# Performance work log

Hardware: AMD Instinct MI355X
Metric: run time of the kernel (lower is better)

The kernel has to match this reference:

```python
import jax, jax.numpy as jnp
import numpy as np

C = 512
M = 8            # n_heads
G = 32           # GroupNorm groups
EPS = 1e-6


def setup_inputs() -> dict:
    key = jax.random.key(0)
    ks = jax.random.split(key, 7)
    x = jax.random.normal(ks[0], (2, C, 64, 64), dtype=jnp.float32)
    gn_weight = jnp.ones((C,), jnp.float32)
    gn_bias = jnp.zeros((C,), jnp.float32)
    qkv_w = jax.random.normal(ks[1], (3 * C, C), jnp.float32) * (1.0 / np.sqrt(C))
    qkv_b = jnp.zeros((3 * C,), jnp.float32)
    # source zero-inits proj_out; we use small random weights so the attention
    proj_w = jax.random.normal(ks[2], (C, C), jnp.float32) * (0.02 / np.sqrt(C))
    proj_b = jnp.zeros((C,), jnp.float32)
    return {"x": x, "gn_weight": gn_weight, "gn_bias": gn_bias,
            "qkv_w": qkv_w, "qkv_b": qkv_b, "proj_w": proj_w, "proj_b": proj_b}


def _forward(x, gn_weight, gn_bias, qkv_w, qkv_b, proj_w, proj_b):
    b, c, H, W = x.shape
    n = H * W
    d = c // M
    xf = x.reshape(b, c, n)

    # GroupNorm(32, c, eps=1e-6, affine)
    xg = xf.reshape(b, G, (c // G) * n)
    mu = xg.mean(axis=-1, keepdims=True)
    var = xg.var(axis=-1, keepdims=True)
    xn = ((xg - mu) * jax.lax.rsqrt(var + EPS)).reshape(b, c, n)
    xn = xn * gn_weight[None, :, None] + gn_bias[None, :, None]

    # 1x1 conv -> qkv, then legacy reshape-then-split
    qkv = jnp.einsum('oc,bcn->bon', qkv_w, xn) + qkv_b[None, :, None]  # (b, 3c, n)
    qkv = qkv.reshape(b * M, 3 * d, n)
    q, k, v = qkv[:, :d], qkv[:, d:2 * d], qkv[:, 2 * d:]

    scale = 1.0 / np.sqrt(np.sqrt(d))
    w = jnp.einsum('Bdi,Bdj->Bij', q * scale, k * scale)  # (b*m, n, n)
    w = jax.nn.softmax(w, axis=-1)
    a = jnp.einsum('Bin,Bdn->Bdi', w, v)                  # (b*m, d, n)
    a = a.reshape(b, c, n)

    h = jnp.einsum('oc,bcn->bon', proj_w, a) + proj_b[None, :, None]
    # NOTE: source reassigns x = norm(x) before the residual add.
    return (xn + h).reshape(b, c, H, W)


def reference(x, gn_weight, gn_bias, qkv_w, qkv_b, proj_w, proj_b):
    return _forward(x, gn_weight, gn_bias, qkv_w, qkv_b, proj_w, proj_b)
```

## Files before the change

### kernel.cpp

```cpp
#include <hip/hip_runtime.h>
#include <cstdint>
#include <cstddef>

typedef __attribute__((ext_vector_type(8))) short short8;
typedef __attribute__((ext_vector_type(4))) float f32x4;

#define QSCALE 0.18033688011112043f

__device__ __forceinline__ float bf2f(unsigned short u) {
  return __uint_as_float(((unsigned)u) << 16);
}
__device__ __forceinline__ unsigned short f2bf(float f) {
  unsigned u = __float_as_uint(f);
  u += 0x7fffu + ((u >> 16) & 1u);
  return (unsigned short)(u >> 16);
}
__device__ __forceinline__ unsigned cvtpk(float a, float b) {
  unsigned r;
  asm("v_cvt_pk_bf16_f32 %0, %1, %2" : "=v"(r) : "v"(a), "v"(b));
  return r;
}
__device__ __forceinline__ short8 mk8(unsigned a, unsigned b, unsigned c, unsigned d) {
  union { unsigned u[4]; short8 s; } x;
  x.u[0] = a; x.u[1] = b; x.u[2] = c; x.u[3] = d;
  return x.s;
}
__device__ __forceinline__ void g2l16(const void* g, void* l) {
  __builtin_amdgcn_global_load_lds(
      (const __attribute__((address_space(1))) unsigned int*)g,
      (__attribute__((address_space(3))) unsigned int*)l, 16, 0, 0);
}

__global__ __launch_bounds__(256) void k_wgn(const float* __restrict__ wqf,
                                             const float* __restrict__ wpf,
                                             unsigned short* __restrict__ wq,
                                             unsigned short* __restrict__ wp,
                                             const float* __restrict__ x,
                                             float* __restrict__ part) {
  __shared__ float red[8];
  const int blk = blockIdx.x;
  const int t = threadIdx.x;
  if (blk < 1024) {
    int i = blk * 256 + t;
    if (i < 196608) {
      float4 v = ((const float4*)wqf)[i];
      ushort4 u;
      u.x = f2bf(v.x); u.y = f2bf(v.y); u.z = f2bf(v.z); u.w = f2bf(v.w);
      ((ushort4*)wq)[i] = u;
    } else {
      int k = i - 196608;
      float4 v = ((const float4*)wpf)[k];
      ushort4 u;
      u.x = f2bf(v.x); u.y = f2bf(v.y); u.z = f2bf(v.z); u.w = f2bf(v.w);
      ((ushort4*)wp)[k] = u;
    }
  } else {
    int b2 = blk - 1024;
    int bg = b2 >> 4, slice = b2 & 15;
    const float4* base = (const float4*)(x + (size_t)bg * 65536 + (size_t)slice * 4096);
    float s = 0.f, q = 0.f;
#pragma unroll
    for (int i = 0; i < 4; ++i) {
      float4 v = base[t + i * 256];
      s += v.x + v.y + v.z + v.w;
      q += v.x * v.x + v.y * v.y + v.z * v.z + v.w * v.w;
    }
#pragma unroll
    for (int off = 1; off < 64; off <<= 1) {
      s += __shfl_xor(s, off);
      q += __shfl_xor(q, off);
    }
    int wid = t >> 6;
    if ((t & 63) == 0) { red[wid * 2] = s; red[wid * 2 + 1] = q; }
    __syncthreads();
    if (t == 0) {
      float S = red[0] + red[2] + red[4] + red[6];
      float Q = red[1] + red[3] + red[5] + red[7];
      part[b2 * 2] = S;
      part[b2 * 2 + 1] = Q;
    }
  }
}

__global__ void k_gnfin(const float* __restrict__ part, float* __restrict__ stats) {
  int t = threadIdx.x;
  float S = 0.f, Q = 0.f;
#pragma unroll
  for (int i = 0; i < 16; ++i) {
    S += part[(t * 16 + i) * 2];
    Q += part[(t * 16 + i) * 2 + 1];
  }
  float mean = S * (1.f / 65536.f);
  float var = Q * (1.f / 65536.f) - mean * mean;
  stats[t * 2] = mean;
  stats[t * 2 + 1] = rsqrtf(var + 1e-6f);
}

__global__ __launch_bounds__(256) void k_gnnorm(const float* __restrict__ x,
                                                const float* __restrict__ gnw,
                                                const float* __restrict__ gnb,
                                                const float* __restrict__ stats,
                                                unsigned short* __restrict__ xn,
                                                unsigned short* __restrict__ xnT) {
  __shared__ float T[64 * 65];
  const int t = threadIdx.x;
  const int n0 = blockIdx.x * 64, c0 = blockIdx.y * 64, bb = blockIdx.z;
#pragma unroll
  for (int p = 0; p < 4; ++p) {
    int s = p * 256 + t;
    int row = s >> 4, seg = s & 15;
    int c = c0 + row;
    int gi = bb * 32 + (c >> 4);
    float mean = stats[gi * 2], rstd = stats[gi * 2 + 1];
    float gw = gnw[c] * rstd;
    float gb = gnb[c] - mean * gw;
    float4 v = *(const float4*)(x + ((size_t)bb * 512 + c) * 4096 + n0 + seg * 4);
    float f0 = v.x * gw + gb, f1 = v.y * gw + gb, f2 = v.z * gw + gb, f3 = v.w * gw + gb;
    ushort4 u;
    u.x = f2bf(f0); u.y = f2bf(f1); u.z = f2bf(f2); u.w = f2bf(f3);
    *(ushort4*)(xn + ((size_t)bb * 512 + c) * 4096 + n0 + seg * 4) = u;
    T[(seg * 4 + 0) * 65 + row] = f0;
    T[(seg * 4 + 1) * 65 + row] = f1;
    T[(seg * 4 + 2) * 65 + row] = f2;
    T[(seg * 4 + 3) * 65 + row] = f3;
  }
  __syncthreads();
#pragma unroll
  for (int p = 0; p < 4; ++p) {
    int s = p * 256 + t;
    int nl = s >> 4, cs = s & 15;
    float f0 = T[nl * 65 + cs * 4 + 0];
    float f1 = T[nl * 65 + cs * 4 + 1];
    float f2 = T[nl * 65 + cs * 4 + 2];
    float f3 = T[nl * 65 + cs * 4 + 3];
    ushort4 u;
    u.x = f2bf(f0); u.y = f2bf(f1); u.z = f2bf(f2); u.w = f2bf(f3);
    *(ushort4*)(xnT + ((size_t)bb * 4096 + n0 + nl) * 512 + c0 + cs * 4) = u;
  }
}

template <int MODE>
__global__ __launch_bounds__(256) void k_gemm(
    const unsigned short* __restrict__ A,
    const unsigned short* __restrict__ Bt,
    const float* __restrict__ bias,
    unsigned short* __restrict__ outA,
    unsigned short* __restrict__ outT,
    const unsigned short* __restrict__ resid,
    float* __restrict__ outF,
    int Mo) {
  __shared__ char lds[34816];
  const int t = threadIdx.x;
  const int lane = t & 63;
  const int g = lane >> 4, ln = lane & 15;
  const int wid = t >> 6, wr = wid >> 1, wc = wid & 1;
  const int bn0 = blockIdx.x * 128, bm0 = blockIdx.y * 128, bb = blockIdx.z;

  const unsigned short* Ab = A + (size_t)bm0 * 512;
  const unsigned short* Bb = Bt + ((size_t)bb * 4096 + bn0) * 512;

  f32x4 acc[4][4];
#pragma unroll
  for (int m = 0; m < 4; ++m)
#pragma unroll
    for (int n = 0; n < 4; ++n) acc[m][n] = f32x4{0.f, 0.f, 0.f, 0.f};

#pragma unroll 1
  for (int kt = 0; kt < 8; ++kt) {
#pragma unroll
    for (int p = 0; p < 4; ++p) {
      int s = p * 256 + t;
      int row = s >> 3;
      int csg = (s & 7) ^ (row & 7);
      g2l16(Ab + (size_t)row * 512 + kt * 64 + csg * 8,
            &lds[(p * 256 + (t & ~63)) * 16]);
    }
#pragma unroll
    for (int p = 0; p < 4; ++p) {
      int s = p * 256 + t;
      int row = s >> 3;
      int csg = (s & 7) ^ (row & 7);
      g2l16(Bb + (size_t)row * 512 + kt * 64 + csg * 8,
            &lds[16384 + (p * 256 + (t & ~63)) * 16]);
    }
    __syncthreads();
#pragma unroll
    for (int kk = 0; kk < 2; ++kk) {
      short8 af[4], bfr[4];
#pragma unroll
      for (int m = 0; m < 4; ++m) {
        int row = wr * 64 + m * 16 + ln;
        int cs = (kk * 4 + g) ^ (row & 7);
        af[m] = *(const short8*)&lds[row * 128 + cs * 16];
      }
#pragma unroll
      for (int n = 0; n < 4; ++n) {
        int row = wc * 64 + n * 16 + ln;
        int cs = (kk * 4 + g) ^ (row & 7);
        bfr[n] = *(const short8*)&lds[16384 + row * 128 + cs * 16];
      }
      __builtin_amdgcn_s_setprio(1);
#pragma unroll
      for (int m = 0; m < 4; ++m)
#pragma unroll
        for (int n = 0; n < 4; ++n)
          acc[m][n] = __builtin_amdgcn_mfma_f32_16x16x32_bf16(af[m], bfr[n], acc[m][n], 0, 0, 0);
      __builtin_amdgcn_s_setprio(0);
    }
    __syncthreads();
  }

  if (MODE == 0) {
#pragma unroll
    for (int m = 0; m < 4; ++m)
#pragma unroll
      for (int n = 0; n < 4; ++n)
#pragma unroll
        for (int r = 0; r < 4; ++r) {
          int ol = wr * 64 + m * 16 + g * 4 + r;
          int jl = wc * 64 + n * 16 + ln;
          int o = bm0 + ol, j = bn0 + jl;
          float v = acc[m][n][r] + bias[o];
          unsigned short bv = f2bf(v);
          if ((o % 192) >= 128) {
            int jp = (j & ~63) | (j & 32) | ((j & 0xC) << 1) | ((j & 16) >> 2) | (j & 3);
            outA[((size_t)bb * 1536 + o) * 4096 + jp] = bv;
          }
          *(unsigned short*)&lds[jl * 272 + ol * 2] = bv;
        }
    __syncthreads();
#pragma unroll
    for (int p = 0; p < 8; ++p) {
      int s = p * 256 + t;
      int jl = s >> 4, cs = s & 15;
      int oo = bm0 + cs * 8;
      if ((oo % 192) < 128) {
        short8 v = *(const short8*)&lds[jl * 272 + cs * 16];
        *(short8*)&outT[((size_t)bb * 4096 + bn0 + jl) * 1536 + oo] = v;
      }
    }
  } else {
#pragma unroll
    for (int m = 0; m < 4; ++m)
#pragma unroll
      for (int n = 0; n < 4; ++n)
#pragma unroll
        for (int r = 0; r < 4; ++r) {
          int o = bm0 + wr * 64 + m * 16 + g * 4 + r;
          int j = bn0 + wc * 64 + n * 16 + ln;
          size_t idx = ((size_t)bb * 512 + o) * 4096 + j;
          outF[idx] = acc[m][n][r] + bias[o] + bf2f(resid[idx]);
        }
  }
}

__global__ __launch_bounds__(512, 4) void k_attn(const unsigned short* __restrict__ qkv,
                                                 const unsigned short* __restrict__ qkvT,
                                                 unsigned short* __restrict__ aT) {
  __shared__ char lds[49152];
  const int t = threadIdx.x, lane = t & 63;
  const int g = lane >> 4, ln = lane & 15;
  const int wid = t >> 6;
  const int qw = wid >> 1;
  const int jw = wid & 1;
  const int h = blockIdx.y, bb = blockIdx.z;
  const int q0 = blockIdx.x * 128 + qw * 32;

  int kaddr[2][2], vaddr[4];
#pragma unroll
  for (int kk = 0; kk < 2; ++kk)
#pragma unroll
    for (int jf = 0; jf < 2; ++jf) {
      int row = jw * 32 + jf * 16 + ln;
      kaddr[kk][jf] = row * 128 + (((kk * 4 + g) ^ (row & 7)) << 4);
    }
#pragma unroll
  for (int df = 0; df < 4; ++df) {
    int row = df * 16 + ln;
    vaddr[df] = 24576 + row * 128 + (((jw * 4 + g) ^ (row & 7)) << 4);
  }

  const unsigned short* kS;
  const unsigned short* vS;
  int ldst;
  {
    int row = t >> 3, csg = (t & 7) ^ (row & 7);
    kS = qkvT + ((size_t)bb * 4096 + row) * 1536 + 192 * h + 64 + csg * 8;
    vS = qkv + ((size_t)bb * 1536 + 192 * h + 128 + row) * 4096 + csg * 8;
    ldst = (t & ~63) * 16;
  }

  short8 qf[2][2];
#pragma unroll
  for (int qt = 0; qt < 2; ++qt)
#pragma unroll
    for (int kk = 0; kk < 2; ++kk) {
      short8 v = *(const short8*)(qkvT + ((size_t)bb * 4096 + q0 + qt * 16 + ln) * 1536 +
                                  192 * h + kk * 32 + g * 8);
#pragma unroll
      for (int e = 0; e < 8; ++e) {
        float f = bf2f((unsigned short)v[e]) * QSCALE;
        v[e] = (short)f2bf(f);
      }
      qf[qt][kk] = v;
    }

  const short8 onesb = mk8(0x3F803F80u, 0x3F803F80u, 0x3F803F80u, 0x3F803F80u);

  f32x4 acc[2][4];
  f32x4 lacc[2];
#pragma unroll
  for (int qt = 0; qt < 2; ++qt) {
#pragma unroll
    for (int df = 0; df < 4; ++df) acc[qt][df] = f32x4{0.f, 0.f, 0.f, 0.f};
    lacc[qt] = f32x4{0.f, 0.f, 0.f, 0.f};
  }

#pragma unroll
  for (int jt = 0; jt < 2; ++jt) {
    g2l16(kS, &lds[jt * 8192 + ldst]);
    g2l16(vS, &lds[24576 + jt * 8192 + ldst]);
    kS += 64 * 1536;
    vS += 64;
  }

#pragma unroll 3
  for (int jt = 0; jt < 64; ++jt) {
    const int cur = jt % 3;
    const char* Kc = &lds[cur * 8192];
    if (jt < 63) {
      asm volatile("s_waitcnt vmcnt(2) lgkmcnt(0)" ::: "memory");
    } else {
      asm volatile("s_waitcnt vmcnt(0) lgkmcnt(0)" ::: "memory");
    }
    __builtin_amdgcn_s_barrier();
    __builtin_amdgcn_sched_barrier(0);

    if (jt < 62) {
      int nb = (jt + 2) % 3;
      g2l16(kS, &lds[nb * 8192 + ldst]);
      g2l16(vS, &lds[24576 + nb * 8192 + ldst]);
      kS += 64 * 1536;
      vS += 64;
    }

    short8 kf[2][2];
#pragma unroll
    for (int kk = 0; kk < 2; ++kk)
#pragma unroll
      for (int jf = 0; jf < 2; ++jf) kf[kk][jf] = *(const short8*)(Kc + kaddr[kk][jf]);

    const f32x4 zf = f32x4{0.f, 0.f, 0.f, 0.f};
    f32x4 w[2][2];
    __builtin_amdgcn_s_setprio(1);
#pragma unroll
    for (int qt = 0; qt < 2; ++qt)
#pragma unroll
      for (int jf = 0; jf < 2; ++jf)
        w[qt][jf] = __builtin_amdgcn_mfma_f32_16x16x32_bf16(kf[0][jf], qf[qt][0], zf, 0, 0, 0);
#pragma unroll
    for (int qt = 0; qt < 2; ++qt)
#pragma unroll
      for (int jf = 0; jf < 2; ++jf)
        w[qt][jf] = __builtin_amdgcn_mfma_f32_16x16x32_bf16(kf[1][jf], qf[qt][1], w[qt][jf], 0, 0, 0);
    __builtin_amdgcn_s_setprio(0);

    short8 vf[4];
#pragma unroll
    for (int df = 0; df < 4; ++df) vf[df] = *(const short8*)(Kc + vaddr[df]);

#pragma unroll
    for (int qt = 0; qt < 2; ++qt)
#pragma unroll
      for (int jf = 0; jf < 2; ++jf)
#pragma unroll
        for (int r = 0; r < 4; ++r) w[qt][jf][r] = __builtin_amdgcn_exp2f(w[qt][jf][r]);

    short8 pf[2];
#pragma unroll
    for (int qt = 0; qt < 2; ++qt)
      pf[qt] = mk8(cvtpk(w[qt][0][0], w[qt][0][1]),
                   cvtpk(w[qt][0][2], w[qt][0][3]),
                   cvtpk(w[qt][1][0], w[qt][1][1]),
                   cvtpk(w[qt][1][2], w[qt][1][3]));

    __builtin_amdgcn_s_setprio(1);
#pragma unroll
    for (int qt = 0; qt < 2; ++qt) {
#pragma unroll
      for (int df = 0; df < 4; ++df)
        acc[qt][df] = __builtin_amdgcn_mfma_f32_16x16x32_bf16(pf[qt], vf[df], acc[qt][df], 0, 0, 0);
      lacc[qt] = __builtin_amdgcn_mfma_f32_16x16x32_bf16(pf[qt], onesb, lacc[qt], 0, 0, 0);
    }
    __builtin_amdgcn_s_setprio(0);
  }

  __syncthreads();
  float* cb = (float*)lds;
  const int cbase = qw * 2560;
  if (jw == 1) {
#pragma unroll
    for (int qt = 0; qt < 2; ++qt) {
#pragma unroll
      for (int df = 0; df < 4; ++df)
        *(f32x4*)&cb[cbase + ((qt * 4 + df) * 64 + lane) * 4] = acc[qt][df];
      *(f32x4*)&cb[cbase + 2048 + (qt * 64 + lane) * 4] = lacc[qt];
    }
  }
  __syncthreads();
  if (jw == 0) {
#pragma unroll
    for (int qt = 0; qt < 2; ++qt) {
#pragma unroll
      for (int df = 0; df < 4; ++df)
        acc[qt][df] += *(const f32x4*)&cb[cbase + ((qt * 4 + df) * 64 + lane) * 4];
      lacc[qt] += *(const f32x4*)&cb[cbase + 2048 + (qt * 64 + lane) * 4];
    }
#pragma unroll
    for (int qt = 0; qt < 2; ++qt)
#pragma unroll
      for (int r = 0; r < 4; ++r) {
        float inv = 1.f / lacc[qt][r];
        int row = q0 + qt * 16 + g * 4 + r;
#pragma unroll
        for (int df = 0; df < 4; ++df)
          aT[((size_t)bb * 4096 + row) * 512 + h * 64 + df * 16 + ln] =
              f2bf(acc[qt][df][r] * inv);
      }
  }
}

extern "C" void kernel_launch(void* const* d_in, const int* in_sizes, int n_in,
                              void* d_out, int out_size, void* d_ws, size_t ws_size,
                              hipStream_t stream) {
  const float* x     = (const float*)d_in[0];
  const float* gnw   = (const float*)d_in[1];
  const float* gnb   = (const float*)d_in[2];
  const float* qkvw  = (const float*)d_in[3];
  const float* qkvb  = (const float*)d_in[4];
  const float* projw = (const float*)d_in[5];
  const float* projb = (const float*)d_in[6];
  float* out = (float*)d_out;
  char* ws = (char*)d_ws;

  const size_t OFF_WQ   = 0;
  const size_t OFF_WP   = 1572864;
  const size_t OFF_XN   = 2097152;
  const size_t OFF_XNT  = 10485760;
  const size_t OFF_QKV  = 18874368;
  const size_t OFF_QKVT = 44040192;
  const size_t OFF_AT   = 69206016;
  const size_t OFF_PART = 77594624;
  const size_t OFF_STAT = 77602816;

  unsigned short* wq   = (unsigned short*)(ws + OFF_WQ);
  unsigned short* wp   = (unsigned short*)(ws + OFF_WP);
  unsigned short* xn   = (unsigned short*)(ws + OFF_XN);
  unsigned short* xnT  = (unsigned short*)(ws + OFF_XNT);
  unsigned short* qkv  = (unsigned short*)(ws + OFF_QKV);
  unsigned short* qkvT = (unsigned short*)(ws + OFF_QKVT);
  unsigned short* aT   = (unsigned short*)(ws + OFF_AT);
  float* part  = (float*)(ws + OFF_PART);
  float* stats = (float*)(ws + OFF_STAT);

  k_wgn<<<dim3(2048), dim3(256), 0, stream>>>(qkvw, projw, wq, wp, x, part);
  k_gnfin<<<dim3(1), dim3(64), 0, stream>>>(part, stats);
  k_gnnorm<<<dim3(64, 8, 2), dim3(256), 0, stream>>>(x, gnw, gnb, stats, xn, xnT);
  k_gemm<0><<<dim3(32, 12, 2), dim3(256), 0, stream>>>(wq, xnT, qkvb, qkv, qkvT, nullptr, nullptr, 1536);
  k_attn<<<dim3(32, 8, 2), dim3(512), 0, stream>>>(qkv, qkvT, aT);
  k_gemm<1><<<dim3(32, 4, 2), dim3(256), 0, stream>>>(wp, aT, projb, nullptr, nullptr, xn, out, 512);
}
```

Baseline: 125.5 us.

## Software-pipeline attention loop: overlap previous tile's PV MFMAs with current exp2

Peels the first key tile into a prologue and restructures the main loop so that each tile's P·V MFMAs run one iteration late, interleaved with the exp2 of the current tile's scores. The aim is to hide transcendental latency behind matrix-core work and stop the MFMA and VALU phases from running back to back. An epilogue drains the last P·V. This keeps more registers live (pf and vfp across iterations), and the interleaving is pinned by sched_barriers, which may constrain the compiler.

Result: slower. 128.0 us (+2.0%).

```diff
diff --git a/kernel.cpp b/kernel.cpp
--- a/kernel.cpp
+++ b/kernel.cpp
@@ -316,6 +316,9 @@
     lacc[qt] = f32x4{0.f, 0.f, 0.f, 0.f};
   }
 
+  short8 pf[2];
+  short8 vfp[4];
+
 #pragma unroll
   for (int jt = 0; jt < 2; ++jt) {
     g2l16(kS, &lds[jt * 8192 + ldst]);
@@ -324,8 +327,52 @@
     vS += 64;
   }
 
+  {
+    asm volatile("s_waitcnt vmcnt(2)" ::: "memory");
+    __builtin_amdgcn_s_barrier();
+    __builtin_amdgcn_sched_barrier(0);
+    g2l16(kS, &lds[2 * 8192 + ldst]);
+    g2l16(vS, &lds[24576 + 2 * 8192 + ldst]);
+    kS += 64 * 1536;
+    vS += 64;
+    const char* Kc = &lds[0];
+    short8 kf[2][2];
+#pragma unroll
+    for (int kk = 0; kk < 2; ++kk)
+#pragma unroll
+      for (int jf = 0; jf < 2; ++jf) kf[kk][jf] = *(const short8*)(Kc + kaddr[kk][jf]);
+    const f32x4 zf = f32x4{0.f, 0.f, 0.f, 0.f};
+    f32x4 w[2][2];
+    __builtin_amdgcn_s_setprio(1);
+#pragma unroll
+    for (int qt = 0; qt < 2; ++qt)
+#pragma unroll
+      for (int jf = 0; jf < 2; ++jf)
+        w[qt][jf] = __builtin_amdgcn_mfma_f32_16x16x32_bf16(kf[0][jf], qf[qt][0], zf, 0, 0, 0);
+#pragma unroll
+    for (int qt = 0; qt < 2; ++qt)
+#pragma unroll
+      for (int jf = 0; jf < 2; ++jf)
+        w[qt][jf] = __builtin_amdgcn_mfma_f32_16x16x32_bf16(kf[1][jf], qf[qt][1], w[qt][jf], 0, 0, 0);
+    __builtin_amdgcn_s_setprio(0);
+#pragma unroll
+    for (int qt = 0; qt < 2; ++qt)
+#pragma unroll
+      for (int jf = 0; jf < 2; ++jf)
+#pragma unroll
+        for (int r = 0; r < 4; ++r) w[qt][jf][r] = __builtin_amdgcn_exp2f(w[qt][jf][r]);
+#pragma unroll
+    for (int qt = 0; qt < 2; ++qt)
+      pf[qt] = mk8(cvtpk(w[qt][0][0], w[qt][0][1]),
+                   cvtpk(w[qt][0][2], w[qt][0][3]),
+                   cvtpk(w[qt][1][0], w[qt][1][1]),
+                   cvtpk(w[qt][1][2], w[qt][1][3]));
+#pragma unroll
+    for (int df = 0; df < 4; ++df) vfp[df] = *(const short8*)(Kc + vaddr[df]);
+  }
+
 #pragma unroll 3
-  for (int jt = 0; jt < 64; ++jt) {
+  for (int jt = 1; jt < 64; ++jt) {
     const int cur = jt % 3;
     const char* Kc = &lds[cur * 8192];
     if (jt < 63) {
@@ -363,37 +410,43 @@
 #pragma unroll
       for (int jf = 0; jf < 2; ++jf)
         w[qt][jf] = __builtin_amdgcn_mfma_f32_16x16x32_bf16(kf[1][jf], qf[qt][1], w[qt][jf], 0, 0, 0);
+    __builtin_amdgcn_sched_barrier(0);
+
+#pragma unroll
+    for (int s = 0; s < 8; ++s) {
+      int pqt = s >> 2, pdf = s & 3;
+      acc[pqt][pdf] =
+          __builtin_amdgcn_mfma_f32_16x16x32_bf16(pf[pqt], vfp[pdf], acc[pqt][pdf], 0, 0, 0);
+      int e0 = 2 * s, e1 = 2 * s + 1;
+      w[e0 >> 3][(e0 >> 2) & 1][e0 & 3] =
+          __builtin_amdgcn_exp2f(w[e0 >> 3][(e0 >> 2) & 1][e0 & 3]);
+      w[e1 >> 3][(e1 >> 2) & 1][e1 & 3] =
+          __builtin_amdgcn_exp2f(w[e1 >> 3][(e1 >> 2) & 1][e1 & 3]);
+      __builtin_amdgcn_sched_barrier(0);
+    }
+    lacc[0] = __builtin_amdgcn_mfma_f32_16x16x32_bf16(pf[0], onesb, lacc[0], 0, 0, 0);
+    lacc[1] = __builtin_amdgcn_mfma_f32_16x16x32_bf16(pf[1], onesb, lacc[1], 0, 0, 0);
+    __builtin_amdgcn_sched_barrier(0);
     __builtin_amdgcn_s_setprio(0);
-
-    short8 vf[4];
-#pragma unroll
-    for (int df = 0; df < 4; ++df) vf[df] = *(const short8*)(Kc + vaddr[df]);
-
-#pragma unroll
-    for (int qt = 0; qt < 2; ++qt)
-#pragma unroll
-      for (int jf = 0; jf < 2; ++jf)
-#pragma unroll
-        for (int r = 0; r < 4; ++r) w[qt][jf][r] = __builtin_amdgcn_exp2f(w[qt][jf][r]);
-
-    short8 pf[2];
 #pragma unroll
     for (int qt = 0; qt < 2; ++qt)
       pf[qt] = mk8(cvtpk(w[qt][0][0], w[qt][0][1]),
                    cvtpk(w[qt][0][2], w[qt][0][3]),
                    cvtpk(w[qt][1][0], w[qt][1][1]),
                    cvtpk(w[qt][1][2], w[qt][1][3]));
-
-    __builtin_amdgcn_s_setprio(1);
-#pragma unroll
-    for (int qt = 0; qt < 2; ++qt) {
-#pragma unroll
-      for (int df = 0; df < 4; ++df)
-        acc[qt][df] = __builtin_amdgcn_mfma_f32_16x16x32_bf16(pf[qt], vf[df], acc[qt][df], 0, 0, 0);
-      lacc[qt] = __builtin_amdgcn_mfma_f32_16x16x32_bf16(pf[qt], onesb, lacc[qt], 0, 0, 0);
-    }
-    __builtin_amdgcn_s_setprio(0);
-  }
+#pragma unroll
+    for (int df = 0; df < 4; ++df) vfp[df] = *(const short8*)(Kc + vaddr[df]);
+  }
+
+  __builtin_amdgcn_s_setprio(1);
+#pragma unroll
+  for (int qt = 0; qt < 2; ++qt) {
+#pragma unroll
+    for (int df = 0; df < 4; ++df)
+      acc[qt][df] = __builtin_amdgcn_mfma_f32_16x16x32_bf16(pf[qt], vfp[df], acc[qt][df], 0, 0, 0);
+    lacc[qt] = __builtin_amdgcn_mfma_f32_16x16x32_bf16(pf[qt], onesb, lacc[qt], 0, 0, 0);
+  }
+  __builtin_amdgcn_s_setprio(0);
 
   __syncthreads();
   float* cb = (float*)lds;
```

## Give each attention wave 64 query rows with half the waves per block

Applied to the files above, without the earlier changes.

The attention kernel now runs 4 waves (256 threads) per block instead of 8. Each wave handles 64 query rows instead of 32, so every K/V fragment read from LDS feeds twice as many MFMAs. Each thread issues two global-to-LDS loads per tile to keep the same 64-row K/V tile, and the wait counts and cross-wave reduction offsets are adjusted to match. The goal is less LDS read traffic per FLOP. The cost is more accumulator registers per wave and fewer waves to hide latency.

Result: no change. 125.0 us (median of 2 runs) (-0.4%).

```diff
diff --git a/kernel.cpp b/kernel.cpp
--- a/kernel.cpp
+++ b/kernel.cpp
@@ -254,7 +254,7 @@
   }
 }
 
-__global__ __launch_bounds__(512, 4) void k_attn(const unsigned short* __restrict__ qkv,
+__global__ __launch_bounds__(256, 2) void k_attn(const unsigned short* __restrict__ qkv,
                                                  const unsigned short* __restrict__ qkvT,
                                                  unsigned short* __restrict__ aT) {
   __shared__ char lds[49152];
@@ -264,7 +264,7 @@
   const int qw = wid >> 1;
   const int jw = wid & 1;
   const int h = blockIdx.y, bb = blockIdx.z;
-  const int q0 = blockIdx.x * 128 + qw * 32;
+  const int q0 = blockIdx.x * 128 + qw * 64;
 
   int kaddr[2][2], vaddr[4];
 #pragma unroll
@@ -280,19 +280,21 @@
     vaddr[df] = 24576 + row * 128 + (((jw * 4 + g) ^ (row & 7)) << 4);
   }
 
-  const unsigned short* kS;
-  const unsigned short* vS;
-  int ldst;
-  {
-    int row = t >> 3, csg = (t & 7) ^ (row & 7);
-    kS = qkvT + ((size_t)bb * 4096 + row) * 1536 + 192 * h + 64 + csg * 8;
-    vS = qkv + ((size_t)bb * 1536 + 192 * h + 128 + row) * 4096 + csg * 8;
-    ldst = (t & ~63) * 16;
-  }
-
-  short8 qf[2][2];
-#pragma unroll
-  for (int qt = 0; qt < 2; ++qt)
+  const unsigned short* kS[2];
+  const unsigned short* vS[2];
+  int ldst[2];
+#pragma unroll
+  for (int p = 0; p < 2; ++p) {
+    int s = p * 256 + t;
+    int row = s >> 3, csg = (s & 7) ^ (row & 7);
+    kS[p] = qkvT + ((size_t)bb * 4096 + row) * 1536 + 192 * h + 64 + csg * 8;
+    vS[p] = qkv + ((size_t)bb * 1536 + 192 * h + 128 + row) * 4096 + csg * 8;
+    ldst[p] = (p * 256 + (t & ~63)) * 16;
+  }
+
+  short8 qf[4][2];
+#pragma unroll
+  for (int qt = 0; qt < 4; ++qt)
 #pragma unroll
     for (int kk = 0; kk < 2; ++kk) {
       short8 v = *(const short8*)(qkvT + ((size_t)bb * 4096 + q0 + qt * 16 + ln) * 1536 +
@@ -307,10 +309,10 @@
 
   const short8 onesb = mk8(0x3F803F80u, 0x3F803F80u, 0x3F803F80u, 0x3F803F80u);
 
-  f32x4 acc[2][4];
-  f32x4 lacc[2];
-#pragma unroll
-  for (int qt = 0; qt < 2; ++qt) {
+  f32x4 acc[4][4];
+  f32x4 lacc[4];
+#pragma unroll
+  for (int qt = 0; qt < 4; ++qt) {
 #pragma unroll
     for (int df = 0; df < 4; ++df) acc[qt][df] = f32x4{0.f, 0.f, 0.f, 0.f};
     lacc[qt] = f32x4{0.f, 0.f, 0.f, 0.f};
@@ -318,10 +320,13 @@
 
 #pragma unroll
   for (int jt = 0; jt < 2; ++jt) {
-    g2l16(kS, &lds[jt * 8192 + ldst]);
-    g2l16(vS, &lds[24576 + jt * 8192 + ldst]);
-    kS += 64 * 1536;
-    vS += 64;
+#pragma unroll
+    for (int p = 0; p < 2; ++p) {
+      g2l16(kS[p], &lds[jt * 8192 + ldst[p]]);
+      g2l16(vS[p], &lds[24576 + jt * 8192 + ldst[p]]);
+      kS[p] += 64 * 1536;
+      vS[p] += 64;
+    }
   }
 
 #pragma unroll 3
@@ -329,7 +334,7 @@
     const int cur = jt % 3;
     const char* Kc = &lds[cur * 8192];
     if (jt < 63) {
-      asm volatile("s_waitcnt vmcnt(2) lgkmcnt(0)" ::: "memory");
+      asm volatile("s_waitcnt vmcnt(4) lgkmcnt(0)" ::: "memory");
     } else {
       asm volatile("s_waitcnt vmcnt(0) lgkmcnt(0)" ::: "memory");
     }
@@ -338,10 +343,13 @@
 
     if (jt < 62) {
       int nb = (jt + 2) % 3;
-      g2l16(kS, &lds[nb * 8192 + ldst]);
-      g2l16(vS, &lds[24576 + nb * 8192 + ldst]);
-      kS += 64 * 1536;
-      vS += 64;
+#pragma unroll
+      for (int p = 0; p < 2; ++p) {
+        g2l16(kS[p], &lds[nb * 8192 + ldst[p]]);
+        g2l16(vS[p], &lds[24576 + nb * 8192 + ldst[p]]);
+        kS[p] += 64 * 1536;
+        vS[p] += 64;
+      }
     }
 
     short8 kf[2][2];
@@ -351,15 +359,15 @@
       for (int jf = 0; jf < 2; ++jf) kf[kk][jf] = *(const short8*)(Kc + kaddr[kk][jf]);
 
     const f32x4 zf = f32x4{0.f, 0.f, 0.f, 0.f};
-    f32x4 w[2][2];
+    f32x4 w[4][2];
     __builtin_amdgcn_s_setprio(1);
 #pragma unroll
-    for (int qt = 0; qt < 2; ++qt)
+    for (int qt = 0; qt < 4; ++qt)
 #pragma unroll
       for (int jf = 0; jf < 2; ++jf)
         w[qt][jf] = __builtin_amdgcn_mfma_f32_16x16x32_bf16(kf[0][jf], qf[qt][0], zf, 0, 0, 0);
 #pragma unroll
-    for (int qt = 0; qt < 2; ++qt)
+    for (int qt = 0; qt < 4; ++qt)
 #pragma unroll
       for (int jf = 0; jf < 2; ++jf)
         w[qt][jf] = __builtin_amdgcn_mfma_f32_16x16x32_bf16(kf[1][jf], qf[qt][1], w[qt][jf], 0, 0, 0);
@@ -370,15 +378,15 @@
     for (int df = 0; df < 4; ++df) vf[df] = *(const short8*)(Kc + vaddr[df]);
 
 #pragma unroll
-    for (int qt = 0; qt < 2; ++qt)
+    for (int qt = 0; qt < 4; ++qt)
 #pragma unroll
       for (int jf = 0; jf < 2; ++jf)
 #pragma unroll
         for (int r = 0; r < 4; ++r) w[qt][jf][r] = __builtin_amdgcn_exp2f(w[qt][jf][r]);
 
-    short8 pf[2];
-#pragma unroll
-    for (int qt = 0; qt < 2; ++qt)
+    short8 pf[4];
+#pragma unroll
+    for (int qt = 0; qt < 4; ++qt)
       pf[qt] = mk8(cvtpk(w[qt][0][0], w[qt][0][1]),
                    cvtpk(w[qt][0][2], w[qt][0][3]),
                    cvtpk(w[qt][1][0], w[qt][1][1]),
@@ -386,7 +394,7 @@
 
     __builtin_amdgcn_s_setprio(1);
 #pragma unroll
-    for (int qt = 0; qt < 2; ++qt) {
+    for (int qt = 0; qt < 4; ++qt) {
 #pragma unroll
       for (int df = 0; df < 4; ++df)
         acc[qt][df] = __builtin_amdgcn_mfma_f32_16x16x32_bf16(pf[qt], vf[df], acc[qt][df], 0, 0, 0);
@@ -397,27 +405,27 @@
 
   __syncthreads();
   float* cb = (float*)lds;
-  const int cbase = qw * 2560;
+  const int cbase = qw * 5120;
   if (jw == 1) {
 #pragma unroll
-    for (int qt = 0; qt < 2; ++qt) {
+    for (int qt = 0; qt < 4; ++qt) {
 #pragma unroll
       for (int df = 0; df < 4; ++df)
         *(f32x4*)&cb[cbase + ((qt * 4 + df) * 64 + lane) * 4] = acc[qt][df];
-      *(f32x4*)&cb[cbase + 2048 + (qt * 64 + lane) * 4] = lacc[qt];
+      *(f32x4*)&cb[cbase + 4096 + (qt * 64 + lane) * 4] = lacc[qt];
     }
   }
   __syncthreads();
   if (jw == 0) {
 #pragma unroll
-    for (int qt = 0; qt < 2; ++qt) {
+    for (int qt = 0; qt < 4; ++qt) {
 #pragma unroll
       for (int df = 0; df < 4; ++df)
         acc[qt][df] += *(const f32x4*)&cb[cbase + ((qt * 4 + df) * 64 + lane) * 4];
-      lacc[qt] += *(const f32x4*)&cb[cbase + 2048 + (qt * 64 + lane) * 4];
-    }
-#pragma unroll
-    for (int qt = 0; qt < 2; ++qt)
+      lacc[qt] += *(const f32x4*)&cb[cbase + 4096 + (qt * 64 + lane) * 4];
+    }
+#pragma unroll
+    for (int qt = 0; qt < 4; ++qt)
 #pragma unroll
       for (int r = 0; r < 4; ++r) {
         float inv = 1.f / lacc[qt][r];
@@ -467,6 +475,6 @@
   k_gnfin<<<dim3(1), dim3(64), 0, stream>>>(part, stats);
   k_gnnorm<<<dim3(64, 8, 2), dim3(256), 0, stream>>>(x, gnw, gnb, stats, xn, xnT);
   k_gemm<0><<<dim3(32, 12, 2), dim3(256), 0, stream>>>(wq, xnT, qkvb, qkv, qkvT, nullptr, nullptr, 1536);
-  k_attn<<<dim3(32, 8, 2), dim3(512), 0, stream>>>(qkv, qkvT, aT);
+  k_attn<<<dim3(32, 8, 2), dim3(256), 0, stream>>>(qkv, qkvT, aT);
   k_gemm<1><<<dim3(32, 4, 2), dim3(256), 0, stream>>>(wp, aT, projb, nullptr, nullptr, xn, out, 512);
 }
```

## Halve attention query tile, double-buffer K/V, and fuse GroupNorm finalize into norm kernel

Applied to the files above, without the earlier changes.

The attention kernel now gives each wave 16 query rows instead of 32 and each block 64 queries instead of 128. It doubles the grid, cuts LDS from 48KB to 32KB, and swaps the 3-stage K/V prefetch ring for a 2-stage double buffer with a full vmcnt(0) wait each iteration. Launch bounds go to 8 waves per SIMD to raise occupancy, but each K/V tile is now reused across half as many queries, so global/LDS traffic per FLOP roughly doubles. Separately, the single-block GroupNorm finalize kernel is removed and each norm block reduces its own 4 group stats into shared memory, saving one launch.

Result: slower. 326.1 us (+159.9%).

```diff
diff --git a/kernel.cpp b/kernel.cpp
--- a/kernel.cpp
+++ b/kernel.cpp
@@ -82,36 +82,36 @@
   }
 }
 
-__global__ void k_gnfin(const float* __restrict__ part, float* __restrict__ stats) {
-  int t = threadIdx.x;
-  float S = 0.f, Q = 0.f;
-#pragma unroll
-  for (int i = 0; i < 16; ++i) {
-    S += part[(t * 16 + i) * 2];
-    Q += part[(t * 16 + i) * 2 + 1];
-  }
-  float mean = S * (1.f / 65536.f);
-  float var = Q * (1.f / 65536.f) - mean * mean;
-  stats[t * 2] = mean;
-  stats[t * 2 + 1] = rsqrtf(var + 1e-6f);
-}
-
 __global__ __launch_bounds__(256) void k_gnnorm(const float* __restrict__ x,
                                                 const float* __restrict__ gnw,
                                                 const float* __restrict__ gnb,
-                                                const float* __restrict__ stats,
+                                                const float* __restrict__ part,
                                                 unsigned short* __restrict__ xn,
                                                 unsigned short* __restrict__ xnT) {
   __shared__ float T[64 * 65];
+  __shared__ float sstats[8];
   const int t = threadIdx.x;
   const int n0 = blockIdx.x * 64, c0 = blockIdx.y * 64, bb = blockIdx.z;
+  if (t < 4) {
+    int gg = bb * 32 + (c0 >> 4) + t;
+    float S = 0.f, Q = 0.f;
+#pragma unroll
+    for (int i = 0; i < 16; ++i) {
+      S += part[(gg * 16 + i) * 2];
+      Q += part[(gg * 16 + i) * 2 + 1];
+    }
+    float mean = S * (1.f / 65536.f);
+    float var = Q * (1.f / 65536.f) - mean * mean;
+    sstats[t * 2] = mean;
+    sstats[t * 2 + 1] = rsqrtf(var + 1e-6f);
+  }
+  __syncthreads();
 #pragma unroll
   for (int p = 0; p < 4; ++p) {
     int s = p * 256 + t;
     int row = s >> 4, seg = s & 15;
     int c = c0 + row;
-    int gi = bb * 32 + (c >> 4);
-    float mean = stats[gi * 2], rstd = stats[gi * 2 + 1];
+    float mean = sstats[(row >> 4) * 2], rstd = sstats[(row >> 4) * 2 + 1];
     float gw = gnw[c] * rstd;
     float gb = gnb[c] - mean * gw;
     float4 v = *(const float4*)(x + ((size_t)bb * 512 + c) * 4096 + n0 + seg * 4);
@@ -254,17 +254,17 @@
   }
 }
 
-__global__ __launch_bounds__(512, 4) void k_attn(const unsigned short* __restrict__ qkv,
+__global__ __launch_bounds__(512, 8) void k_attn(const unsigned short* __restrict__ qkv,
                                                  const unsigned short* __restrict__ qkvT,
                                                  unsigned short* __restrict__ aT) {
-  __shared__ char lds[49152];
+  __shared__ char lds[32768];
   const int t = threadIdx.x, lane = t & 63;
   const int g = lane >> 4, ln = lane & 15;
   const int wid = t >> 6;
   const int qw = wid >> 1;
   const int jw = wid & 1;
   const int h = blockIdx.y, bb = blockIdx.z;
-  const int q0 = blockIdx.x * 128 + qw * 32;
+  const int q0 = blockIdx.x * 64 + qw * 16;
 
   int kaddr[2][2], vaddr[4];
 #pragma unroll
@@ -277,7 +277,7 @@
 #pragma unroll
   for (int df = 0; df < 4; ++df) {
     int row = df * 16 + ln;
-    vaddr[df] = 24576 + row * 128 + (((jw * 4 + g) ^ (row & 7)) << 4);
+    vaddr[df] = 8192 + row * 128 + (((jw * 4 + g) ^ (row & 7)) << 4);
   }
 
   const unsigned short* kS;
@@ -290,56 +290,42 @@
     ldst = (t & ~63) * 16;
   }
 
-  short8 qf[2][2];
-#pragma unroll
-  for (int qt = 0; qt < 2; ++qt)
-#pragma unroll
-    for (int kk = 0; kk < 2; ++kk) {
-      short8 v = *(const short8*)(qkvT + ((size_t)bb * 4096 + q0 + qt * 16 + ln) * 1536 +
-                                  192 * h + kk * 32 + g * 8);
-#pragma unroll
-      for (int e = 0; e < 8; ++e) {
-        float f = bf2f((unsigned short)v[e]) * QSCALE;
-        v[e] = (short)f2bf(f);
-      }
-      qf[qt][kk] = v;
-    }
+  short8 qf[2];
+#pragma unroll
+  for (int kk = 0; kk < 2; ++kk) {
+    short8 v = *(const short8*)(qkvT + ((size_t)bb * 4096 + q0 + ln) * 1536 +
+                                192 * h + kk * 32 + g * 8);
+#pragma unroll
+    for (int e = 0; e < 8; ++e) {
+      float f = bf2f((unsigned short)v[e]) * QSCALE;
+      v[e] = (short)f2bf(f);
+    }
+    qf[kk] = v;
+  }
 
   const short8 onesb = mk8(0x3F803F80u, 0x3F803F80u, 0x3F803F80u, 0x3F803F80u);
 
-  f32x4 acc[2][4];
-  f32x4 lacc[2];
-#pragma unroll
-  for (int qt = 0; qt < 2; ++qt) {
-#pragma unroll
-    for (int df = 0; df < 4; ++df) acc[qt][df] = f32x4{0.f, 0.f, 0.f, 0.f};
-    lacc[qt] = f32x4{0.f, 0.f, 0.f, 0.f};
-  }
-
-#pragma unroll
-  for (int jt = 0; jt < 2; ++jt) {
-    g2l16(kS, &lds[jt * 8192 + ldst]);
-    g2l16(vS, &lds[24576 + jt * 8192 + ldst]);
-    kS += 64 * 1536;
-    vS += 64;
-  }
-
-#pragma unroll 3
+  f32x4 acc[4];
+  f32x4 lacc = f32x4{0.f, 0.f, 0.f, 0.f};
+#pragma unroll
+  for (int df = 0; df < 4; ++df) acc[df] = f32x4{0.f, 0.f, 0.f, 0.f};
+
+  g2l16(kS, &lds[ldst]);
+  g2l16(vS, &lds[8192 + ldst]);
+  kS += 64 * 1536;
+  vS += 64;
+
+#pragma unroll 2
   for (int jt = 0; jt < 64; ++jt) {
-    const int cur = jt % 3;
-    const char* Kc = &lds[cur * 8192];
-    if (jt < 63) {
-      asm volatile("s_waitcnt vmcnt(2) lgkmcnt(0)" ::: "memory");
-    } else {
-      asm volatile("s_waitcnt vmcnt(0) lgkmcnt(0)" ::: "memory");
-    }
+    const int cur = jt & 1;
+    const char* B = &lds[cur * 16384];
+    asm volatile("s_waitcnt vmcnt(0) lgkmcnt(0)" ::: "memory");
     __builtin_amdgcn_s_barrier();
     __builtin_amdgcn_sched_barrier(0);
 
-    if (jt < 62) {
-      int nb = (jt + 2) % 3;
-      g2l16(kS, &lds[nb * 8192 + ldst]);
-      g2l16(vS, &lds[24576 + nb * 8192 + ldst]);
+    if (jt < 63) {
+      g2l16(kS, &lds[(cur ^ 1) * 16384 + ldst]);
+      g2l16(vS, &lds[(cur ^ 1) * 16384 + 8192 + ldst]);
       kS += 64 * 1536;
       vS += 64;
     }
@@ -348,85 +334,63 @@
 #pragma unroll
     for (int kk = 0; kk < 2; ++kk)
 #pragma unroll
-      for (int jf = 0; jf < 2; ++jf) kf[kk][jf] = *(const short8*)(Kc + kaddr[kk][jf]);
+      for (int jf = 0; jf < 2; ++jf) kf[kk][jf] = *(const short8*)(B + kaddr[kk][jf]);
 
     const f32x4 zf = f32x4{0.f, 0.f, 0.f, 0.f};
-    f32x4 w[2][2];
+    f32x4 w[2];
     __builtin_amdgcn_s_setprio(1);
 #pragma unroll
-    for (int qt = 0; qt < 2; ++qt)
-#pragma unroll
-      for (int jf = 0; jf < 2; ++jf)
-        w[qt][jf] = __builtin_amdgcn_mfma_f32_16x16x32_bf16(kf[0][jf], qf[qt][0], zf, 0, 0, 0);
-#pragma unroll
-    for (int qt = 0; qt < 2; ++qt)
-#pragma unroll
-      for (int jf = 0; jf < 2; ++jf)
-        w[qt][jf] = __builtin_amdgcn_mfma_f32_16x16x32_bf16(kf[1][jf], qf[qt][1], w[qt][jf], 0, 0, 0);
+    for (int jf = 0; jf < 2; ++jf)
+      w[jf] = __builtin_amdgcn_mfma_f32_16x16x32_bf16(kf[0][jf], qf[0], zf, 0, 0, 0);
+#pragma unroll
+    for (int jf = 0; jf < 2; ++jf)
+      w[jf] = __builtin_amdgcn_mfma_f32_16x16x32_bf16(kf[1][jf], qf[1], w[jf], 0, 0, 0);
     __builtin_amdgcn_s_setprio(0);
 
     short8 vf[4];
 #pragma unroll
-    for (int df = 0; df < 4; ++df) vf[df] = *(const short8*)(Kc + vaddr[df]);
-
-#pragma unroll
-    for (int qt = 0; qt < 2; ++qt)
-#pragma unroll
-      for (int jf = 0; jf < 2; ++jf)
-#pragma unroll
-        for (int r = 0; r < 4; ++r) w[qt][jf][r] = __builtin_amdgcn_exp2f(w[qt][jf][r]);
-
-    short8 pf[2];
-#pragma unroll
-    for (int qt = 0; qt < 2; ++qt)
-      pf[qt] = mk8(cvtpk(w[qt][0][0], w[qt][0][1]),
-                   cvtpk(w[qt][0][2], w[qt][0][3]),
-                   cvtpk(w[qt][1][0], w[qt][1][1]),
-                   cvtpk(w[qt][1][2], w[qt][1][3]));
+    for (int df = 0; df < 4; ++df) vf[df] = *(const short8*)(B + vaddr[df]);
+
+#pragma unroll
+    for (int jf = 0; jf < 2; ++jf)
+#pragma unroll
+      for (int r = 0; r < 4; ++r) w[jf][r] = __builtin_amdgcn_exp2f(w[jf][r]);
+
+    short8 pf = mk8(cvtpk(w[0][0], w[0][1]), cvtpk(w[0][2], w[0][3]),
+                    cvtpk(w[1][0], w[1][1]), cvtpk(w[1][2], w[1][3]));
 
     __builtin_amdgcn_s_setprio(1);
 #pragma unroll
-    for (int qt = 0; qt < 2; ++qt) {
-#pragma unroll
-      for (int df = 0; df < 4; ++df)
-        acc[qt][df] = __builtin_amdgcn_mfma_f32_16x16x32_bf16(pf[qt], vf[df], acc[qt][df], 0, 0, 0);
-      lacc[qt] = __builtin_amdgcn_mfma_f32_16x16x32_bf16(pf[qt], onesb, lacc[qt], 0, 0, 0);
-    }
+    for (int df = 0; df < 4; ++df)
+      acc[df] = __builtin_amdgcn_mfma_f32_16x16x32_bf16(pf, vf[df], acc[df], 0, 0, 0);
+    lacc = __builtin_amdgcn_mfma_f32_16x16x32_bf16(pf, onesb, lacc, 0, 0, 0);
     __builtin_amdgcn_s_setprio(0);
   }
 
   __syncthreads();
   float* cb = (float*)lds;
-  const int cbase = qw * 2560;
+  const int cbase = qw * 1280;
   if (jw == 1) {
 #pragma unroll
-    for (int qt = 0; qt < 2; ++qt) {
-#pragma unroll
-      for (int df = 0; df < 4; ++df)
-        *(f32x4*)&cb[cbase + ((qt * 4 + df) * 64 + lane) * 4] = acc[qt][df];
-      *(f32x4*)&cb[cbase + 2048 + (qt * 64 + lane) * 4] = lacc[qt];
-    }
+    for (int df = 0; df < 4; ++df)
+      *(f32x4*)&cb[cbase + (df * 64 + lane) * 4] = acc[df];
+    *(f32x4*)&cb[cbase + 1024 + lane * 4] = lacc;
   }
   __syncthreads();
   if (jw == 0) {
 #pragma unroll
-    for (int qt = 0; qt < 2; ++qt) {
+    for (int df = 0; df < 4; ++df)
+      acc[df] += *(const f32x4*)&cb[cbase + (df * 64 + lane) * 4];
+    lacc += *(const f32x4*)&cb[cbase + 1024 + lane * 4];
+#pragma unroll
+    for (int r = 0; r < 4; ++r) {
+      float inv = 1.f / lacc[r];
+      int row = q0 + g * 4 + r;
 #pragma unroll
       for (int df = 0; df < 4; ++df)
-        acc[qt][df] += *(const f32x4*)&cb[cbase + ((qt * 4 + df) * 64 + lane) * 4];
-      lacc[qt] += *(const f32x4*)&cb[cbase + 2048 + (qt * 64 + lane) * 4];
-    }
-#pragma unroll
-    for (int qt = 0; qt < 2; ++qt)
-#pragma unroll
-      for (int r = 0; r < 4; ++r) {
-        float inv = 1.f / lacc[qt][r];
-        int row = q0 + qt * 16 + g * 4 + r;
-#pragma unroll
-        for (int df = 0; df < 4; ++df)
-          aT[((size_t)bb * 4096 + row) * 512 + h * 64 + df * 16 + ln] =
-              f2bf(acc[qt][df][r] * inv);
-      }
+        aT[((size_t)bb * 4096 + row) * 512 + h * 64 + df * 16 + ln] =
+            f2bf(acc[df][r] * inv);
+    }
   }
 }
 
@@ -451,7 +415,6 @@
   const size_t OFF_QKVT = 44040192;
   const size_t OFF_AT   = 69206016;
   const size_t OFF_PART = 77594624;
-  const size_t OFF_STAT = 77602816;
 
   unsigned short* wq   = (unsigned short*)(ws + OFF_WQ);
   unsigned short* wp   = (unsigned short*)(ws + OFF_WP);
@@ -461,12 +424,10 @@
   unsigned short* qkvT = (unsigned short*)(ws + OFF_QKVT);
   unsigned short* aT   = (unsigned short*)(ws + OFF_AT);
   float* part  = (float*)(ws + OFF_PART);
-  float* stats = (float*)(ws + OFF_STAT);
 
   k_wgn<<<dim3(2048), dim3(256), 0, stream>>>(qkvw, projw, wq, wp, x, part);
-  k_gnfin<<<dim3(1), dim3(64), 0, stream>>>(part, stats);
-  k_gnnorm<<<dim3(64, 8, 2), dim3(256), 0, stream>>>(x, gnw, gnb, stats, xn, xnT);
+  k_gnnorm<<<dim3(64, 8, 2), dim3(256), 0, stream>>>(x, gnw, gnb, part, xn, xnT);
   k_gemm<0><<<dim3(32, 12, 2), dim3(256), 0, stream>>>(wq, xnT, qkvb, qkv, qkvT, nullptr, nullptr, 1536);
-  k_attn<<<dim3(32, 8, 2), dim3(512), 0, stream>>>(qkv, qkvT, aT);
+  k_attn<<<dim3(64, 8, 2), dim3(512), 0, stream>>>(qkv, qkvT, aT);
   k_gemm<1><<<dim3(32, 4, 2), dim3(256), 0, stream>>>(wp, aT, projb, nullptr, nullptr, xn, out, 512);
 }
```
